# Kernel tuning notes

Measured on AMD Instinct MI355X. Metric: run time of the kernel, lower is better.

The kernel has to match this reference:

```python
import jax, jax.numpy as jnp
import numpy as np

RESOLUTION = 2 ** 8  # 256
N_POINTS = 2 ** 21


def setup_inputs() -> dict:
    key = jax.random.key(0)
    k1, k2 = jax.random.split(key)
    inp = jax.random.uniform(k1, (N_POINTS, 3), dtype=jnp.float32)
    grid = jax.random.normal(k2, (RESOLUTION, RESOLUTION, RESOLUTION, 3), dtype=jnp.float32) * 0.01
    return {"input": inp, "feature_params": grid}


def reference(input, feature_params):
    R = feature_params.shape[0]
    scaled = input * (R - 1)
    lower = jnp.clip(jnp.floor(scaled).astype(jnp.int32), 0, R - 2)
    upper = jnp.clip(lower + 1, 0, R - 1)
    t = scaled - lower.astype(scaled.dtype)
    xl, yl, zl = lower[:, 0], lower[:, 1], lower[:, 2]
    xu, yu, zu = upper[:, 0], upper[:, 1], upper[:, 2]
    tx, ty, tz = t[:, 0:1], t[:, 1:2], t[:, 2:3]  # (N,1) for broadcast over channels
    # note original indexes grid as [z, y, x]
    c000 = feature_params[zl, yl, xl]
    c001 = feature_params[zl, yl, xu]
    c010 = feature_params[zl, yu, xl]
    c011 = feature_params[zl, yu, xu]
    c100 = feature_params[zu, yl, xl]
    c101 = feature_params[zu, yl, xu]
    c110 = feature_params[zu, yu, xl]
    c111 = feature_params[zu, yu, xu]
    c00 = c000 * (1 - tx) + c001 * tx
    c01 = c010 * (1 - tx) + c011 * tx
    c10 = c100 * (1 - tx) + c101 * tx
    c11 = c110 * (1 - tx) + c111 * tx
    c0 = c00 * (1 - ty) + c01 * ty
    c1 = c10 * (1 - ty) + c11 * ty
    return c0 * (1 - tz) + c1 * tz
```

## Files before the change

### kernel.cpp

```cpp
#include <hip/hip_runtime.h>


#define NB     8192
#define GBLK   512
#define CHUNKF 100
#define NCHUNK 81
#define NF4    2025
#define LDSF   8100

#define OFF_OFF   33554432u
#define CUR_OFF   (33554432u + 32772u)
#define HIST_OFF  (33554432u + 32772u + 32768u)
#define NEEDED    (33554432u + 32772u + 32768u + 32768u)

typedef float f4v __attribute__((ext_vector_type(4)));
typedef float f2v __attribute__((ext_vector_type(2)));
typedef f4v f4u __attribute__((aligned(8)));
typedef f2v f2u __attribute__((aligned(8)));

__device__ __forceinline__ void cell_of(float p, int& l, float& t) {
    float s = p * 255.0f;
    int v = (int)floorf(s);
    v = v < 0 ? 0 : (v > 254 ? 254 : v);
    l = v;
    t = s - (float)v;
}

__device__ __forceinline__ int fine_bin3(float px, float py, float pz) {
    int xl, yl, zl; float tx, ty, tz;
    cell_of(px, xl, tx);
    cell_of(py, yl, ty);
    cell_of(pz, zl, tz);
    return ((zl >> 3) << 8) | ((yl >> 3) << 3) | (xl >> 5);
}

__global__ __launch_bounds__(1024) void k_zero(unsigned* __restrict__ hist) {
    int i = blockIdx.x * 1024 + threadIdx.x;
    if (i < NB) hist[i] = 0;
}

__global__ __launch_bounds__(1024) void k_hist(const float* __restrict__ inp,
                                               unsigned* __restrict__ hist, int n) {
    __shared__ unsigned h[NB];
    int t = threadIdx.x;
    for (int i = t; i < NB; i += 1024) h[i] = 0;
    __syncthreads();
    int P = n >> 1;
    int stride = gridDim.x * 1024;
    for (int pr = blockIdx.x * 1024 + t; pr < P; pr += stride) {
        f4v a = *(const f4u*)(inp + 6 * pr);
        f2v b = *(const f2u*)(inp + 6 * pr + 4);
        atomicAdd(&h[fine_bin3(a.x, a.y, a.z)], 1u);
        atomicAdd(&h[fine_bin3(a.w, b.x, b.y)], 1u);
    }
    if ((n & 1) && blockIdx.x == 0 && t == 0) {
        int i = n - 1;
        atomicAdd(&hist[fine_bin3(inp[3 * i], inp[3 * i + 1], inp[3 * i + 2])], 1u);
    }
    __syncthreads();
    for (int i = t; i < NB; i += 1024)
        if (h[i]) atomicAdd(&hist[i], h[i]);
}

__global__ __launch_bounds__(1024) void k_scan(const unsigned* __restrict__ hist,
                                               unsigned* __restrict__ off,
                                               unsigned* __restrict__ cur) {
    __shared__ unsigned s[1024];
    int t = threadIdx.x;
    unsigned v[8];
    unsigned sum = 0;
#pragma unroll
    for (int k = 0; k < 8; ++k) { v[k] = hist[8 * t + k]; sum += v[k]; }
    s[t] = sum;
    __syncthreads();
    for (int d = 1; d < 1024; d <<= 1) {
        unsigned add = (t >= d) ? s[t - d] : 0u;
        __syncthreads();
        s[t] += add;
        __syncthreads();
    }
    unsigned e = s[t] - sum;
#pragma unroll
    for (int k = 0; k < 8; ++k) {
        off[8 * t + k] = e;
        cur[8 * t + k] = e;
        e += v[k];
    }
    if (t == 1023) off[NB] = s[1023];
}

__global__ __launch_bounds__(1024) void k_scatter(const float* __restrict__ inp,
                                                  float4* __restrict__ binned,
                                                  unsigned* __restrict__ cur, int n) {
    __shared__ unsigned cnt[NB];
    __shared__ unsigned base[NB];
    int t = threadIdx.x;
    int P = n >> 1;
    int stride = gridDim.x * 1024;
    int iters = (P + stride - 1) / stride;

    if ((n & 1) && blockIdx.x == 0 && t == 0) {
        int i = n - 1;
        float px = inp[3 * i], py = inp[3 * i + 1], pz = inp[3 * i + 2];
        int b = fine_bin3(px, py, pz);
        unsigned r = atomicAdd(&cur[b], 1u);
        float4 v; v.x = px; v.y = py; v.z = pz; v.w = __uint_as_float((unsigned)i);
        binned[r] = v;
    }

    for (int it = 0; it < iters; ++it) {
        int pr = it * stride + blockIdx.x * 1024 + t;
        for (int k = t; k < NB; k += 1024) cnt[k] = 0;
        __syncthreads();
        int b0 = 0, b1 = 0; unsigned r0 = 0, r1 = 0;
        float4 p0, p1;
        bool valid = (pr < P);
        if (valid) {
            f4v a = *(const f4u*)(inp + 6 * pr);
            f2v b = *(const f2u*)(inp + 6 * pr + 4);
            p0.x = a.x; p0.y = a.y; p0.z = a.z;
            p0.w = __uint_as_float((unsigned)(2 * pr));
            p1.x = a.w; p1.y = b.x; p1.z = b.y;
            p1.w = __uint_as_float((unsigned)(2 * pr + 1));
            b0 = fine_bin3(p0.x, p0.y, p0.z);
            b1 = fine_bin3(p1.x, p1.y, p1.z);
            r0 = atomicAdd(&cnt[b0], 1u);
            r1 = atomicAdd(&cnt[b1], 1u);
        }
        __syncthreads();
        for (int k = t; k < NB; k += 1024)
            if (cnt[k]) base[k] = atomicAdd(&cur[k], cnt[k]);
        __syncthreads();
        if (valid) {
            binned[base[b0] + r0] = p0;
            binned[base[b1] + r1] = p1;
        }
        __syncthreads();
    }
}

__global__ __launch_bounds__(GBLK, 8) void k_gather(const float4* __restrict__ binned,
                                                    const float* __restrict__ grid,
                                                    const unsigned* __restrict__ off,
                                                    float* __restrict__ out) {
    __shared__ __align__(16) float slab[LDSF];
    int bin = blockIdx.x;
    int x0 = (bin & 7) << 5;
    int y0 = ((bin >> 3) & 31) << 3;
    int z0 = (bin >> 8) << 3;
    int t = threadIdx.x;

    unsigned start = off[bin], end = off[bin + 1];
    unsigned count = end - start;

    float4 v;
    if ((unsigned)t < count) v = binned[start + (unsigned)t];

    for (int u = t; u < NF4; u += GBLK) {
        int chunk = u / 25;
        int j = u - chunk * 25;
        int zc = chunk / 9;
        int yc = chunk - zc * 9;
        int zg = z0 + zc; zg = zg > 255 ? 255 : zg;
        int yg = y0 + yc; yg = yg > 255 ? 255 : yg;
        int joff = (j == 24 && x0 == 224) ? 0 : (j << 2);
        const float* src = grid + (size_t)((zg << 16) | (yg << 8) | x0) * 3 + joff;
        __builtin_amdgcn_global_load_lds(
            (const __attribute__((address_space(1))) unsigned int*)src,
            (__attribute__((address_space(3))) unsigned int*)&slab[(size_t)u * 4],
            16, 0, 0);
    }
    __syncthreads();

    unsigned p = (unsigned)t;
    while (p < count) {
        float px = v.x, py = v.y, pz = v.z;
        unsigned idx = __float_as_uint(v.w);
        p += (unsigned)GBLK;
        if (p < count) v = binned[start + p];

        int xl, yl, zl; float tx, ty, tz;
        cell_of(px, xl, tx);
        cell_of(py, yl, ty);
        cell_of(pz, zl, tz);
        int xc = xl - x0, yc = yl - y0, zc = zl - z0;

        int r0 = (zc * 9 + yc) * CHUNKF + xc * 3;
        int e = r0 & ~1;
        bool d = (r0 & 1) != 0;

#define SEG_READ(b, s)                                   \
        do {                                             \
            f2v q0 = *(const f2u*)(&slab[(b)]);          \
            f2v q1 = *(const f2u*)(&slab[(b) + 2]);      \
            f2v q2 = *(const f2u*)(&slab[(b) + 4]);      \
            f2v q3 = *(const f2u*)(&slab[(b) + 6]);      \
            s[0] = d ? q0.y : q0.x;                      \
            s[1] = d ? q1.x : q0.y;                      \
            s[2] = d ? q1.y : q1.x;                      \
            s[3] = d ? q2.x : q1.y;                      \
            s[4] = d ? q2.y : q2.x;                      \
            s[5] = d ? q3.x : q2.y;                      \
        } while (0)

        float s00[6], s01[6], s10[6], s11[6];
        SEG_READ(e,               s00);
        SEG_READ(e + CHUNKF,      s01);
        SEG_READ(e + 9 * CHUNKF,  s10);
        SEG_READ(e + 10 * CHUNKF, s11);
#undef SEG_READ

        float o[3];
#pragma unroll
        for (int c = 0; c < 3; ++c) {
            float c00 = s00[c] * (1.0f - tx) + s00[c + 3] * tx;
            float c01 = s01[c] * (1.0f - tx) + s01[c + 3] * tx;
            float c10 = s10[c] * (1.0f - tx) + s10[c + 3] * tx;
            float c11 = s11[c] * (1.0f - tx) + s11[c + 3] * tx;
            float c0 = c00 * (1.0f - ty) + c01 * ty;
            float c1 = c10 * (1.0f - ty) + c11 * ty;
            o[c] = c0 * (1.0f - tz) + c1 * tz;
        }
        float3 w; w.x = o[0]; w.y = o[1]; w.z = o[2];
        *(float3*)(out + 3 * (size_t)idx) = w;
    }
}

__global__ __launch_bounds__(256) void k_direct(const float* __restrict__ inp,
                                                const float* __restrict__ grid,
                                                float* __restrict__ out, int n) {
    int i = blockIdx.x * blockDim.x + threadIdx.x;
    if (i >= n) return;
    int xl, yl, zl; float tx, ty, tz;
    cell_of(inp[3 * i + 0], xl, tx);
    cell_of(inp[3 * i + 1], yl, ty);
    cell_of(inp[3 * i + 2], zl, tz);
    int b00 = (zl * 65536 + yl * 256 + xl) * 3;
    int b01 = b00 + 768, b10 = b00 + 196608, b11 = b10 + 768;
    float s00[6], s01[6], s10[6], s11[6];
#pragma unroll
    for (int kk = 0; kk < 6; ++kk) s00[kk] = grid[b00 + kk];
#pragma unroll
    for (int kk = 0; kk < 6; ++kk) s01[kk] = grid[b01 + kk];
#pragma unroll
    for (int kk = 0; kk < 6; ++kk) s10[kk] = grid[b10 + kk];
#pragma unroll
    for (int kk = 0; kk < 6; ++kk) s11[kk] = grid[b11 + kk];
#pragma unroll
    for (int c = 0; c < 3; ++c) {
        float c00 = s00[c] * (1.0f - tx) + s00[c + 3] * tx;
        float c01 = s01[c] * (1.0f - tx) + s01[c + 3] * tx;
        float c10 = s10[c] * (1.0f - tx) + s10[c + 3] * tx;
        float c11 = s11[c] * (1.0f - tx) + s11[c + 3] * tx;
        float c0 = c00 * (1.0f - ty) + c01 * ty;
        float c1 = c10 * (1.0f - ty) + c11 * ty;
        out[3 * i + c] = c0 * (1.0f - tz) + c1 * tz;
    }
}

extern "C" void kernel_launch(void* const* d_in, const int* in_sizes, int n_in,
                              void* d_out, int out_size, void* d_ws, size_t ws_size,
                              hipStream_t stream) {
    const float* inp  = (const float*)d_in[0];
    const float* grid = (const float*)d_in[1];
    float* out = (float*)d_out;
    int n = in_sizes[0] / 3;

    if (ws_size < (size_t)NEEDED) {
        int blocks = (n + 255) / 256;
        k_direct<<<blocks, 256, 0, stream>>>(inp, grid, out, n);
        return;
    }

    char* ws = (char*)d_ws;
    float4*   binned = (float4*)ws;
    unsigned* off    = (unsigned*)(ws + OFF_OFF);
    unsigned* cur    = (unsigned*)(ws + CUR_OFF);
    unsigned* hist   = (unsigned*)(ws + HIST_OFF);

    k_zero   <<<8,   1024, 0, stream>>>(hist);
    k_hist   <<<256, 1024, 0, stream>>>(inp, hist, n);
    k_scan   <<<1,   1024, 0, stream>>>(hist, off, cur);
    k_scatter<<<256, 1024, 0, stream>>>(inp, binned, cur, n);
    k_gather <<<NB,  GBLK, 0, stream>>>(binned, grid, off, out);
}
```

Before: 146.9 us.

## Replace histogram+scan with fixed-capacity bins and direct overflow fallback

Removes the histogram and prefix-scan kernels by giving each of the 8192 bins a fixed slot capacity of 512, so the scatter pass writes straight into preallocated regions. Points that overflow a bin are interpolated directly in the scatter kernel with global loads. The gather kernel reads its count from the cursor array, and its block-to-bin mapping is permuted to interleave bins. This saves a full read pass over the input and two launches, at the cost of a larger workspace and a slow path if bins overflow.

```diff
diff --git a/kernel.cpp b/kernel.cpp
--- a/kernel.cpp
+++ b/kernel.cpp
@@ -2,16 +2,15 @@
 
 
 #define NB     8192
+#define CAP    512u
 #define GBLK   512
 #define CHUNKF 100
 #define NCHUNK 81
 #define NF4    2025
 #define LDSF   8100
 
-#define OFF_OFF   33554432u
-#define CUR_OFF   (33554432u + 32772u)
-#define HIST_OFF  (33554432u + 32772u + 32768u)
-#define NEEDED    (33554432u + 32772u + 32768u + 32768u)
+#define CUR_OFF   67108864u
+#define NEEDED    (67108864u + 32768u)
 
 typedef float f4v __attribute__((ext_vector_type(4)));
 typedef float f2v __attribute__((ext_vector_type(2)));
@@ -34,64 +33,43 @@
     return ((zl >> 3) << 8) | ((yl >> 3) << 3) | (xl >> 5);
 }
 
-__global__ __launch_bounds__(1024) void k_zero(unsigned* __restrict__ hist) {
+__device__ __forceinline__ void direct_lerp(const float* __restrict__ grid,
+                                            float* __restrict__ out, int i,
+                                            int xl, int yl, int zl,
+                                            float tx, float ty, float tz) {
+    int b00 = (zl * 65536 + yl * 256 + xl) * 3;
+    int b01 = b00 + 768, b10 = b00 + 196608, b11 = b10 + 768;
+    float s00[6], s01[6], s10[6], s11[6];
+#pragma unroll
+    for (int k = 0; k < 6; ++k) s00[k] = grid[b00 + k];
+#pragma unroll
+    for (int k = 0; k < 6; ++k) s01[k] = grid[b01 + k];
+#pragma unroll
+    for (int k = 0; k < 6; ++k) s10[k] = grid[b10 + k];
+#pragma unroll
+    for (int k = 0; k < 6; ++k) s11[k] = grid[b11 + k];
+#pragma unroll
+    for (int c = 0; c < 3; ++c) {
+        float c00 = s00[c] * (1.0f - tx) + s00[c + 3] * tx;
+        float c01 = s01[c] * (1.0f - tx) + s01[c + 3] * tx;
+        float c10 = s10[c] * (1.0f - tx) + s10[c + 3] * tx;
+        float c11 = s11[c] * (1.0f - tx) + s11[c + 3] * tx;
+        float c0 = c00 * (1.0f - ty) + c01 * ty;
+        float c1 = c10 * (1.0f - ty) + c11 * ty;
+        out[3 * i + c] = c0 * (1.0f - tz) + c1 * tz;
+    }
+}
+
+__global__ __launch_bounds__(1024) void k_init(unsigned* __restrict__ cur) {
     int i = blockIdx.x * 1024 + threadIdx.x;
-    if (i < NB) hist[i] = 0;
-}
-
-__global__ __launch_bounds__(1024) void k_hist(const float* __restrict__ inp,
-                                               unsigned* __restrict__ hist, int n) {
-    __shared__ unsigned h[NB];
-    int t = threadIdx.x;
-    for (int i = t; i < NB; i += 1024) h[i] = 0;
-    __syncthreads();
-    int P = n >> 1;
-    int stride = gridDim.x * 1024;
-    for (int pr = blockIdx.x * 1024 + t; pr < P; pr += stride) {
-        f4v a = *(const f4u*)(inp + 6 * pr);
-        f2v b = *(const f2u*)(inp + 6 * pr + 4);
-        atomicAdd(&h[fine_bin3(a.x, a.y, a.z)], 1u);
-        atomicAdd(&h[fine_bin3(a.w, b.x, b.y)], 1u);
-    }
-    if ((n & 1) && blockIdx.x == 0 && t == 0) {
-        int i = n - 1;
-        atomicAdd(&hist[fine_bin3(inp[3 * i], inp[3 * i + 1], inp[3 * i + 2])], 1u);
-    }
-    __syncthreads();
-    for (int i = t; i < NB; i += 1024)
-        if (h[i]) atomicAdd(&hist[i], h[i]);
-}
-
-__global__ __launch_bounds__(1024) void k_scan(const unsigned* __restrict__ hist,
-                                               unsigned* __restrict__ off,
-                                               unsigned* __restrict__ cur) {
-    __shared__ unsigned s[1024];
-    int t = threadIdx.x;
-    unsigned v[8];
-    unsigned sum = 0;
-#pragma unroll
-    for (int k = 0; k < 8; ++k) { v[k] = hist[8 * t + k]; sum += v[k]; }
-    s[t] = sum;
-    __syncthreads();
-    for (int d = 1; d < 1024; d <<= 1) {
-        unsigned add = (t >= d) ? s[t - d] : 0u;
-        __syncthreads();
-        s[t] += add;
-        __syncthreads();
-    }
-    unsigned e = s[t] - sum;
-#pragma unroll
-    for (int k = 0; k < 8; ++k) {
-        off[8 * t + k] = e;
-        cur[8 * t + k] = e;
-        e += v[k];
-    }
-    if (t == 1023) off[NB] = s[1023];
+    if (i < NB) cur[i] = (unsigned)i * CAP;
 }
 
 __global__ __launch_bounds__(1024) void k_scatter(const float* __restrict__ inp,
+                                                  const float* __restrict__ grid,
                                                   float4* __restrict__ binned,
-                                                  unsigned* __restrict__ cur, int n) {
+                                                  unsigned* __restrict__ cur,
+                                                  float* __restrict__ out, int n) {
     __shared__ unsigned cnt[NB];
     __shared__ unsigned base[NB];
     int t = threadIdx.x;
@@ -104,8 +82,14 @@
         float px = inp[3 * i], py = inp[3 * i + 1], pz = inp[3 * i + 2];
         int b = fine_bin3(px, py, pz);
         unsigned r = atomicAdd(&cur[b], 1u);
-        float4 v; v.x = px; v.y = py; v.z = pz; v.w = __uint_as_float((unsigned)i);
-        binned[r] = v;
+        if (r - (unsigned)b * CAP < CAP) {
+            float4 v; v.x = px; v.y = py; v.z = pz; v.w = __uint_as_float((unsigned)i);
+            binned[r] = v;
+        } else {
+            int xl, yl, zl; float tx, ty, tz;
+            cell_of(px, xl, tx); cell_of(py, yl, ty); cell_of(pz, zl, tz);
+            direct_lerp(grid, out, i, xl, yl, zl, tx, ty, tz);
+        }
     }
 
     for (int it = 0; it < iters; ++it) {
@@ -132,8 +116,20 @@
             if (cnt[k]) base[k] = atomicAdd(&cur[k], cnt[k]);
         __syncthreads();
         if (valid) {
-            binned[base[b0] + r0] = p0;
-            binned[base[b1] + r1] = p1;
+            unsigned s0 = base[b0] + r0;
+            unsigned s1 = base[b1] + r1;
+            if (s0 - (unsigned)b0 * CAP < CAP) binned[s0] = p0;
+            else {
+                int xl, yl, zl; float tx, ty, tz;
+                cell_of(p0.x, xl, tx); cell_of(p0.y, yl, ty); cell_of(p0.z, zl, tz);
+                direct_lerp(grid, out, 2 * pr, xl, yl, zl, tx, ty, tz);
+            }
+            if (s1 - (unsigned)b1 * CAP < CAP) binned[s1] = p1;
+            else {
+                int xl, yl, zl; float tx, ty, tz;
+                cell_of(p1.x, xl, tx); cell_of(p1.y, yl, ty); cell_of(p1.z, zl, tz);
+                direct_lerp(grid, out, 2 * pr + 1, xl, yl, zl, tx, ty, tz);
+            }
         }
         __syncthreads();
     }
@@ -141,17 +137,18 @@
 
 __global__ __launch_bounds__(GBLK, 8) void k_gather(const float4* __restrict__ binned,
                                                     const float* __restrict__ grid,
-                                                    const unsigned* __restrict__ off,
+                                                    const unsigned* __restrict__ cur,
                                                     float* __restrict__ out) {
     __shared__ __align__(16) float slab[LDSF];
-    int bin = blockIdx.x;
+    int bin = ((blockIdx.x & 7) << 10) | (blockIdx.x >> 3);
     int x0 = (bin & 7) << 5;
     int y0 = ((bin >> 3) & 31) << 3;
     int z0 = (bin >> 8) << 3;
     int t = threadIdx.x;
 
-    unsigned start = off[bin], end = off[bin + 1];
-    unsigned count = end - start;
+    unsigned start = (unsigned)bin * CAP;
+    unsigned count = cur[bin] - start;
+    if (count > CAP) count = CAP;
 
     float4 v;
     if ((unsigned)t < count) v = binned[start + (unsigned)t];
@@ -235,27 +232,7 @@
     cell_of(inp[3 * i + 0], xl, tx);
     cell_of(inp[3 * i + 1], yl, ty);
     cell_of(inp[3 * i + 2], zl, tz);
-    int b00 = (zl * 65536 + yl * 256 + xl) * 3;
-    int b01 = b00 + 768, b10 = b00 + 196608, b11 = b10 + 768;
-    float s00[6], s01[6], s10[6], s11[6];
-#pragma unroll
-    for (int kk = 0; kk < 6; ++kk) s00[kk] = grid[b00 + kk];
-#pragma unroll
-    for (int kk = 0; kk < 6; ++kk) s01[kk] = grid[b01 + kk];
-#pragma unroll
-    for (int kk = 0; kk < 6; ++kk) s10[kk] = grid[b10 + kk];
-#pragma unroll
-    for (int kk = 0; kk < 6; ++kk) s11[kk] = grid[b11 + kk];
-#pragma unroll
-    for (int c = 0; c < 3; ++c) {
-        float c00 = s00[c] * (1.0f - tx) + s00[c + 3] * tx;
-        float c01 = s01[c] * (1.0f - tx) + s01[c + 3] * tx;
-        float c10 = s10[c] * (1.0f - tx) + s10[c + 3] * tx;
-        float c11 = s11[c] * (1.0f - tx) + s11[c + 3] * tx;
-        float c0 = c00 * (1.0f - ty) + c01 * ty;
-        float c1 = c10 * (1.0f - ty) + c11 * ty;
-        out[3 * i + c] = c0 * (1.0f - tz) + c1 * tz;
-    }
+    direct_lerp(grid, out, i, xl, yl, zl, tx, ty, tz);
 }
 
 extern "C" void kernel_launch(void* const* d_in, const int* in_sizes, int n_in,
@@ -274,13 +251,9 @@
 
     char* ws = (char*)d_ws;
     float4*   binned = (float4*)ws;
-    unsigned* off    = (unsigned*)(ws + OFF_OFF);
     unsigned* cur    = (unsigned*)(ws + CUR_OFF);
-    unsigned* hist   = (unsigned*)(ws + HIST_OFF);
-
-    k_zero   <<<8,   1024, 0, stream>>>(hist);
-    k_hist   <<<256, 1024, 0, stream>>>(inp, hist, n);
-    k_scan   <<<1,   1024, 0, stream>>>(hist, off, cur);
-    k_scatter<<<256, 1024, 0, stream>>>(inp, binned, cur, n);
-    k_gather <<<NB,  GBLK, 0, stream>>>(binned, grid, off, out);
-}
+
+    k_init   <<<8,   1024, 0, stream>>>(cur);
+    k_scatter<<<256, 1024, 0, stream>>>(inp, grid, binned, cur, out, n);
+    k_gather <<<NB,  GBLK, 0, stream>>>(binned, grid, cur, out);
+}
```

Result: faster. 141.4 us (-3.8%).
